# Optimization experiments

Measured on AMD Instinct MI355X. Metric: run time of the kernel, lower is better.

The kernel has to match this reference:

```python
import jax, jax.numpy as jnp
import numpy as np

NUM_GRAPHS = 128
EPS = 1e-5


def _instance_norm(x, seg, num_seg):
    # Per-graph instance norm over rows grouped by seg (PyG InstanceNorm, affine=False).
    ones = jnp.ones((x.shape[0], 1), x.dtype)
    cnt = jnp.maximum(jax.ops.segment_sum(ones, seg, num_segments=num_seg), 1.0)  # [G,1]
    mean = jax.ops.segment_sum(x, seg, num_segments=num_seg) / cnt               # [G,C]
    xc = x - mean[seg]
    var = jax.ops.segment_sum(xc * xc, seg, num_segments=num_seg) / cnt          # [G,C]
    return xc * jax.lax.rsqrt(var[seg] + EPS)


def setup_inputs() -> dict:
    key = jax.random.key(0)
    ks = jax.random.split(key, 8)
    N, E, H, G = 50000, 800000, 64, NUM_GRAPHS
    emb = jax.random.normal(ks[0], (N, H), dtype=jnp.float32)
    edge_index = jax.random.randint(ks[1], (2, E), 0, N, dtype=jnp.int64)
    batch = jnp.sort(jax.random.randint(ks[2], (N,), 0, G, dtype=jnp.int64))
    s1 = 1.0 / np.sqrt(2 * H)
    s2 = 1.0 / np.sqrt(4 * H)
    s3 = 1.0 / np.sqrt(H)
    return {
        "emb": emb,
        "edge_index": edge_index,
        "batch": batch,
        "W1": jax.random.normal(ks[3], (2 * H, 4 * H), dtype=jnp.float32) * s1,
        "b1": jnp.zeros((4 * H,), jnp.float32),
        "W2": jax.random.normal(ks[4], (4 * H, H), dtype=jnp.float32) * s2,
        "b2": jnp.zeros((H,), jnp.float32),
        "W3": jax.random.normal(ks[5], (H, 1), dtype=jnp.float32) * s3,
        "b3": jnp.zeros((1,), jnp.float32),
    }


def reference(emb, edge_index, batch, W1, b1, W2, b2, W3, b3):
    col, row = edge_index[0], edge_index[1]
    # Gather both endpoint embeddings and concat: [E, 2H]
    f12 = jnp.concatenate([emb[col], emb[row]], axis=-1)
    seg = batch[col]  # graph id per edge
    # MLP([2H, 4H, H, 1]): Linear -> InstanceNorm(batch) -> ReLU (dropout=identity in eval)
    h = jnp.maximum(_instance_norm(f12 @ W1 + b1, seg, NUM_GRAPHS), 0.0)
    h = jnp.maximum(_instance_norm(h @ W2 + b2, seg, NUM_GRAPHS), 0.0)
    att_log_logits = h @ W3 + b3  # [E, 1]
    return att_log_logits
```

## Files before the change

### kernel.cpp

```cpp
#include <hip/hip_runtime.h>
#include <hip/hip_bf16.h>
#include <stdint.h>

#define NG 128
#define EPSI 1e-5f

typedef __attribute__((ext_vector_type(8))) __bf16 bf16x8;
typedef __attribute__((ext_vector_type(4))) float f32x4;

union ABFrag { bf16x8 v; unsigned short u[8]; uint4 q; };
union U8 { uint4 q; unsigned short u[8]; };

__device__ __forceinline__ float b2f(unsigned short u){
  union { unsigned int i; float f; } v; v.i = ((unsigned int)u) << 16; return v.f;
}
__device__ __forceinline__ unsigned short f2b(float f){
  union { float f; unsigned int i; } v; v.f = f;
  unsigned int r = v.i + 0x7fffu + ((v.i >> 16) & 1u);
  return (unsigned short)(r >> 16);
}
__device__ __forceinline__ unsigned int pk2(float lo, float hi){
  unsigned int r;
  asm("v_cvt_pk_bf16_f32 %0, %1, %2" : "=v"(r) : "v"(lo), "v"(hi));
  return r;
}

__global__ void kprep(const float* __restrict__ emb, const float* __restrict__ W1,
                      const float* __restrict__ W2,
                      const int* __restrict__ ei, const int* __restrict__ batch,
                      unsigned short* __restrict__ embb, unsigned short* __restrict__ WcF,
                      unsigned short* __restrict__ W2F, unsigned int* __restrict__ hist,
                      unsigned int* __restrict__ nodeh, int N, int E){
  __shared__ unsigned int h[NG];
  for (int i = threadIdx.x; i < NG; i += 256) h[i] = 0;
  __syncthreads();
  int idx = blockIdx.x * 256 + threadIdx.x;
  int stride = gridDim.x * 256;
  int embCnt4 = N * 16;
  for (int i = idx; i < embCnt4; i += stride){
    float4 v = *(const float4*)(emb + (size_t)i * 4);
    ushort4 o; o.x = f2b(v.x); o.y = f2b(v.y); o.z = f2b(v.z); o.w = f2b(v.w);
    *(ushort4*)(embb + (size_t)i * 4) = o;
  }
  for (int i = idx; i < 32 * 2 * 64 * 8; i += stride){
    int j = i & 7, lane = (i >> 3) & 63, ks = (i >> 9) & 1, tn = i >> 10;
    int quad = lane >> 4, l15 = lane & 15;
    int k = ks * 32 + quad * 8 + j;
    int n = tn * 16 + l15;
    float wv = (n < 256) ? W1[k * 256 + n] : W1[(k + 64) * 256 + (n - 256)];
    WcF[i] = f2b(wv);
  }
  for (int i = idx; i < 4 * 8 * 64 * 8; i += stride){
    int j = i & 7, lane = (i >> 3) & 63, ks = (i >> 9) & 7, w = i >> 12;
    int quad = lane >> 4, l15 = lane & 15;
    W2F[i] = f2b(W2[(ks * 32 + quad * 8 + j) * 64 + w * 16 + l15]);
  }
  for (int e = idx; e < E; e += stride){
    int cn = ei[e];
    atomicAdd(&h[batch[cn]], 1u);
    atomicAdd(&nodeh[cn], 1u);
  }
  __syncthreads();
  for (int i = threadIdx.x; i < NG; i += 256)
    if (h[i]) atomicAdd(&hist[i], h[i]);
}

__global__ void __launch_bounds__(256) kscan(const unsigned int* __restrict__ nodeh,
                      const unsigned int* __restrict__ hist,
                      const int* __restrict__ batch,
                      unsigned int* __restrict__ ncursor,
                      unsigned int* __restrict__ gmeta, int N){
  __shared__ unsigned int sh[3];
  __shared__ unsigned int wtot[4];
  int g = blockIdx.x;
  int t = threadIdx.x;
  unsigned int part = 0;
  for (int i = t; i < g; i += 256) part += (hist[i] + 31u) & ~31u;
  #pragma unroll
  for (int d = 1; d < 64; d <<= 1) part += __shfl_xor(part, d);
  if ((t & 63) == 0) wtot[t >> 6] = part;
  if (t == 64 || t == 65){
    int target = g + (t - 64);
    int lo = 0, hi = N;
    while (lo < hi){ int mid = (lo + hi) >> 1; if (batch[mid] < target) lo = mid + 1; else hi = mid; }
    sh[1 + (t - 64)] = lo;
  }
  __syncthreads();
  if (t == 0){
    unsigned int pb = wtot[0] + wtot[1] + wtot[2] + wtot[3];
    sh[0] = pb;
    gmeta[g] = pb;
    if (g == NG - 1) gmeta[NG] = pb + ((hist[g] + 31u) & ~31u);
  }
  __syncthreads();
  unsigned int run = sh[0];
  int lo = (int)sh[1], hi = (int)sh[2];
  int wid = t >> 6;
  for (int base = lo; base < hi; base += 256){
    int i = base + t;
    unsigned int v = (i < hi) ? nodeh[i] : 0u;
    unsigned int x = v;
    #pragma unroll
    for (int d = 1; d < 64; d <<= 1){
      unsigned int y = __shfl_up(x, d);
      if ((t & 63) >= d) x += y;
    }
    if ((t & 63) == 63) wtot[wid] = x;
    __syncthreads();
    unsigned int woff = 0;
    #pragma unroll
    for (int wb = 0; wb < 4; ++wb) if (wb < wid) woff += wtot[wb];
    if (i < hi) ncursor[i] = run + woff + x - v;
    run += wtot[0] + wtot[1] + wtot[2] + wtot[3];
    __syncthreads();
  }
}

__global__ void kscatter(const int* __restrict__ ei, const int* __restrict__ batch, int E,
                         unsigned int* __restrict__ ncursor, int4* __restrict__ einfo){
  int idx = blockIdx.x * 256 + threadIdx.x;
  for (int e = idx; e < E; e += gridDim.x * 256){
    int cn = ei[e], rn = ei[E + e];
    int g = batch[cn];
    unsigned int p = atomicAdd(&ncursor[cn], 1u);
    einfo[p] = make_int4(cn, rn, g, e);
  }
}

__global__ void kpad(int4* __restrict__ einfo, const unsigned int* __restrict__ hist,
                     const unsigned int* __restrict__ gmeta){
  int g = blockIdx.x;
  unsigned int cnt = hist[g];
  if (!cnt) return;
  unsigned int pe = (cnt + 31u) & ~31u;
  if (cnt == pe) return;
  unsigned int base = gmeta[g];
  int4 e0 = einfo[base]; e0.w = -1;
  for (unsigned int i = cnt + threadIdx.x; i < pe; i += 64)
    einfo[base + i] = e0;
}

__global__ void __launch_bounds__(256) kgemm1(const unsigned short* __restrict__ embb,
    const unsigned short* __restrict__ WcF, const float* __restrict__ b1,
    unsigned short* __restrict__ PQb, int Nn){
  int wave = threadIdx.x >> 6, lane = threadIdx.x & 63;
  int quad = lane >> 4, l15 = lane & 15;
  int tm = blockIdx.x * 4 + wave;
  int tmmax = (Nn + 15) >> 4;
  if (tm >= tmmax) return;
  int m = tm * 16 + l15; if (m >= Nn) m = Nn - 1;
  ABFrag a0, a1;
  a0.q = *(const uint4*)(embb + (size_t)m * 64 + quad * 8);
  a1.q = *(const uint4*)(embb + (size_t)m * 64 + 32 + quad * 8);
  int rowbase = tm * 16 + quad * 4;
  #pragma unroll 4
  for (int tn = 0; tn < 32; ++tn){
    ABFrag b0, b1f;
    b0.q  = *(const uint4*)(WcF + ((size_t)(tn * 2 + 0) * 64 + lane) * 8);
    b1f.q = *(const uint4*)(WcF + ((size_t)(tn * 2 + 1) * 64 + lane) * 8);
    f32x4 acc = {0.f, 0.f, 0.f, 0.f};
    acc = __builtin_amdgcn_mfma_f32_16x16x32_bf16(a0.v, b0.v, acc, 0, 0, 0);
    acc = __builtin_amdgcn_mfma_f32_16x16x32_bf16(a1.v, b1f.v, acc, 0, 0, 0);
    int col = tn * 16 + l15;
    float bias = (col < 256) ? b1[col] : 0.0f;
    #pragma unroll
    for (int r = 0; r < 4; ++r){
      int rowg = rowbase + r;
      if (rowg < Nn) PQb[(size_t)rowg * 512 + col] = f2b(acc[r] + bias);
    }
  }
}

__global__ void __launch_bounds__(256) kstats1(const unsigned short* __restrict__ PQb,
    const int4* __restrict__ einfo, const int* __restrict__ batch,
    const unsigned int* __restrict__ ncursor, const unsigned int* __restrict__ nodeh,
    float* __restrict__ sum1, float* __restrict__ sq1, int N){
  __shared__ float lsum[4][256];
  __shared__ float lsq[4][256];
  int tid = threadIdx.x;
  for (int i = tid; i < 4 * 256; i += 256){ ((float*)lsum)[i] = 0.f; ((float*)lsq)[i] = 0.f; }
  __syncthreads();
  int base = blockIdx.x * 32;
  int gfirst = batch[base];
  int wid = tid >> 6, lane = tid & 63;
  int c4 = lane * 4;
  float T1[4] = {0.f,0.f,0.f,0.f}, T2[4] = {0.f,0.f,0.f,0.f};
  int curg = -1;
  auto flushT = [&](){
    if (curg >= 0){
      unsigned slot = (unsigned)(curg - gfirst);
      if (slot < 4u){
        #pragma unroll
        for (int t = 0; t < 4; ++t){
          atomicAdd(&lsum[slot][c4 + t], T1[t]);
          atomicAdd(&lsq[slot][c4 + t], T2[t]);
        }
      } else {
        #pragma unroll
        for (int t = 0; t < 4; ++t){
          atomicAdd(&sum1[curg * 256 + c4 + t], T1[t]);
          atomicAdd(&sq1[curg * 256 + c4 + t], T2[t]);
        }
      }
      #pragma unroll
      for (int t = 0; t < 4; ++t){ T1[t] = 0.f; T2[t] = 0.f; }
    }
  };
  for (int i = 0; i < 8; ++i){
    int n = base + wid + i * 4;
    if (n >= N) break;
    int g = batch[n];
    unsigned int cnt = nodeh[n];
    if (g != curg){ flushT(); curg = g; }
    if (!cnt) continue;
    unsigned int start = ncursor[n] - cnt;
    ushort4 pv = *(const ushort4*)(PQb + (size_t)n * 512 + c4);
    float S1[4] = {0.f,0.f,0.f,0.f}, S2[4] = {0.f,0.f,0.f,0.f};
    for (unsigned int jb = 0; jb < cnt; jb += 64){
      int jn = (int)min(64u, cnt - jb);
      int rnv = (lane < jn) ? einfo[start + jb + (unsigned)lane].y : 0;
      #pragma unroll 4
      for (int j = 0; j < jn; ++j){
        int rn = __shfl(rnv, j);
        ushort4 qv = *(const ushort4*)(PQb + (size_t)rn * 512 + 256 + c4);
        float q0 = b2f(qv.x), q1 = b2f(qv.y), q2 = b2f(qv.z), q3 = b2f(qv.w);
        S1[0] += q0; S2[0] = fmaf(q0, q0, S2[0]);
        S1[1] += q1; S2[1] = fmaf(q1, q1, S2[1]);
        S1[2] += q2; S2[2] = fmaf(q2, q2, S2[2]);
        S1[3] += q3; S2[3] = fmaf(q3, q3, S2[3]);
      }
    }
    float fc = (float)cnt;
    float p0 = b2f(pv.x), p1 = b2f(pv.y), p2 = b2f(pv.z), p3 = b2f(pv.w);
    T1[0] += fmaf(fc, p0, S1[0]);  T2[0] += fmaf(fmaf(fc, p0, 2.f * S1[0]), p0, S2[0]);
    T1[1] += fmaf(fc, p1, S1[1]);  T2[1] += fmaf(fmaf(fc, p1, 2.f * S1[1]), p1, S2[1]);
    T1[2] += fmaf(fc, p2, S1[2]);  T2[2] += fmaf(fmaf(fc, p2, 2.f * S1[2]), p2, S2[2]);
    T1[3] += fmaf(fc, p3, S1[3]);  T2[3] += fmaf(fmaf(fc, p3, 2.f * S1[3]), p3, S2[3]);
  }
  flushT();
  __syncthreads();
  for (int i = tid; i < 4 * 256; i += 256){
    int slot = i >> 8, ch = i & 255;
    float vs = lsum[slot][ch], vq = lsq[slot][ch];
    if (vs != 0.f || vq != 0.f){
      int g = gfirst + slot;
      atomicAdd(&sum1[g * 256 + ch], vs);
      atomicAdd(&sq1[g * 256 + ch], vq);
    }
  }
}

__global__ void kfin(const float* __restrict__ sum, const float* __restrict__ sq,
                     const unsigned int* __restrict__ hist,
                     float* __restrict__ meanA, float* __restrict__ rstdA,
                     float* __restrict__ mrA, int C){
  int i = blockIdx.x * blockDim.x + threadIdx.x;
  if (i >= NG * C) return;
  int g = i / C;
  float cnt = fmaxf((float)hist[g], 1.0f);
  float m = sum[i] / cnt;
  float v = sq[i] / cnt - m * m;
  float r = rsqrtf(fmaxf(v, 0.f) + EPSI);
  meanA[i] = m;
  rstdA[i] = r;
  mrA[i] = m * r;
}

__global__ void __launch_bounds__(256, 5) kmain(const unsigned short* __restrict__ PQb,
    const unsigned short* __restrict__ W2F, const int4* __restrict__ einfo,
    const float* __restrict__ rstd1, const float* __restrict__ mr1,
    const float* __restrict__ b2,
    const unsigned int* __restrict__ hist, const unsigned int* __restrict__ gmeta,
    unsigned short* __restrict__ y2b, float* __restrict__ sum2, float* __restrict__ sq2){
  __shared__ unsigned short Blds[4 * 8 * 64 * 8];
  {
    const uint4* src = (const uint4*)W2F;
    uint4* dst = (uint4*)Blds;
    for (int i = threadIdx.x; i < 2048; i += 256) dst[i] = src[i];
  }
  __syncthreads();
  int wave = threadIdx.x >> 6, lane = threadIdx.x & 63;
  int quad = lane >> 4, l15 = lane & 15;
  float b2v[4];
  #pragma unroll
  for (int cg = 0; cg < 4; ++cg) b2v[cg] = b2[cg * 16 + l15];
  int ntiles = (int)(gmeta[NG] >> 5);
  int nw = gridDim.x * 4;
  for (int t = blockIdx.x * 4 + wave; t < ntiles; t += nw){
    int p0 = t * 32;
    int4 ev0 = einfo[p0 + l15];
    int4 ev1 = einfo[p0 + 16 + l15];
    int g = __builtin_amdgcn_readfirstlane(ev0.z);
    const unsigned short* pp0 = PQb + (size_t)ev0.x * 512 + quad * 8;
    const unsigned short* qq0 = PQb + (size_t)ev0.y * 512 + 256 + quad * 8;
    const unsigned short* pp1 = PQb + (size_t)ev1.x * 512 + quad * 8;
    const unsigned short* qq1 = PQb + (size_t)ev1.y * 512 + 256 + quad * 8;
    const float* rr = rstd1 + g * 256 + quad * 8;
    const float* mm = mr1   + g * 256 + quad * 8;
    f32x4 acc[8];
    #pragma unroll
    for (int i = 0; i < 8; ++i){ acc[i][0]=0.f; acc[i][1]=0.f; acc[i][2]=0.f; acc[i][3]=0.f; }
    #pragma unroll 2
    for (int ks = 0; ks < 8; ++ks){
      U8 pu0, qu0, pu1, qu1;
      pu0.q = *(const uint4*)(pp0 + ks * 32);
      qu0.q = *(const uint4*)(qq0 + ks * 32);
      pu1.q = *(const uint4*)(pp1 + ks * 32);
      qu1.q = *(const uint4*)(qq1 + ks * 32);
      float4 ra = *(const float4*)(rr + ks * 32);
      float4 rb = *(const float4*)(rr + ks * 32 + 4);
      float4 ma = *(const float4*)(mm + ks * 32);
      float4 mb = *(const float4*)(mm + ks * 32 + 4);
      float s00 = b2f(pu0.u[0]) + b2f(qu0.u[0]);
      float s01 = b2f(pu0.u[1]) + b2f(qu0.u[1]);
      float s02 = b2f(pu0.u[2]) + b2f(qu0.u[2]);
      float s03 = b2f(pu0.u[3]) + b2f(qu0.u[3]);
      float s04 = b2f(pu0.u[4]) + b2f(qu0.u[4]);
      float s05 = b2f(pu0.u[5]) + b2f(qu0.u[5]);
      float s06 = b2f(pu0.u[6]) + b2f(qu0.u[6]);
      float s07 = b2f(pu0.u[7]) + b2f(qu0.u[7]);
      float s10 = b2f(pu1.u[0]) + b2f(qu1.u[0]);
      float s11 = b2f(pu1.u[1]) + b2f(qu1.u[1]);
      float s12 = b2f(pu1.u[2]) + b2f(qu1.u[2]);
      float s13 = b2f(pu1.u[3]) + b2f(qu1.u[3]);
      float s14 = b2f(pu1.u[4]) + b2f(qu1.u[4]);
      float s15 = b2f(pu1.u[5]) + b2f(qu1.u[5]);
      float s16 = b2f(pu1.u[6]) + b2f(qu1.u[6]);
      float s17 = b2f(pu1.u[7]) + b2f(qu1.u[7]);
      ABFrag a0, a1;
      a0.q.x = pk2(fmaxf(0.f, fmaf(s00, ra.x, -ma.x)), fmaxf(0.f, fmaf(s01, ra.y, -ma.y)));
      a0.q.y = pk2(fmaxf(0.f, fmaf(s02, ra.z, -ma.z)), fmaxf(0.f, fmaf(s03, ra.w, -ma.w)));
      a0.q.z = pk2(fmaxf(0.f, fmaf(s04, rb.x, -mb.x)), fmaxf(0.f, fmaf(s05, rb.y, -mb.y)));
      a0.q.w = pk2(fmaxf(0.f, fmaf(s06, rb.z, -mb.z)), fmaxf(0.f, fmaf(s07, rb.w, -mb.w)));
      a1.q.x = pk2(fmaxf(0.f, fmaf(s10, ra.x, -ma.x)), fmaxf(0.f, fmaf(s11, ra.y, -ma.y)));
      a1.q.y = pk2(fmaxf(0.f, fmaf(s12, ra.z, -ma.z)), fmaxf(0.f, fmaf(s13, ra.w, -ma.w)));
      a1.q.z = pk2(fmaxf(0.f, fmaf(s14, rb.x, -mb.x)), fmaxf(0.f, fmaf(s15, rb.y, -mb.y)));
      a1.q.w = pk2(fmaxf(0.f, fmaf(s16, rb.z, -mb.z)), fmaxf(0.f, fmaf(s17, rb.w, -mb.w)));
      #pragma unroll
      for (int cg = 0; cg < 4; ++cg){
        ABFrag b;
        b.q = *(const uint4*)&Blds[((cg * 8 + ks) * 64 + lane) * 8];
        acc[cg]     = __builtin_amdgcn_mfma_f32_16x16x32_bf16(a0.v, b.v, acc[cg], 0, 0, 0);
        acc[4 + cg] = __builtin_amdgcn_mfma_f32_16x16x32_bf16(a1.v, b.v, acc[4 + cg], 0, 0, 0);
      }
    }
    int nl = (int)gmeta[g] + (int)hist[g] - p0;
    #pragma unroll
    for (int cg = 0; cg < 4; ++cg){
      float s = 0.f, qs = 0.f;
      #pragma unroll
      for (int sub = 0; sub < 2; ++sub)
        #pragma unroll
        for (int r = 0; r < 4; ++r){
          float y = acc[sub * 4 + cg][r] + b2v[cg];
          int el = sub * 16 + quad * 4 + r;
          y2b[(size_t)(p0 + el) * 64 + cg * 16 + l15] = f2b(y);
          if (el < nl){ s += y; qs = fmaf(y, y, qs); }
        }
      s  += __shfl_xor(s, 16);  s  += __shfl_xor(s, 32);
      qs += __shfl_xor(qs, 16); qs += __shfl_xor(qs, 32);
      if (quad == 0){
        atomicAdd(&sum2[g * 64 + cg * 16 + l15], s);
        atomicAdd(&sq2[g * 64 + cg * 16 + l15], qs);
      }
    }
  }
}

__global__ void kfinal(const unsigned short* __restrict__ y2b, const int4* __restrict__ einfo,
                       const unsigned int* __restrict__ gmeta,
                       const float* __restrict__ mean2, const float* __restrict__ rstd2,
                       const float* __restrict__ W3, const float* __restrict__ b3,
                       float* __restrict__ out){
  int EP = (int)gmeta[NG];
  int sub = threadIdx.x & 7;
  int c8 = sub * 8;
  float w3r[8];
  #pragma unroll
  for (int t = 0; t < 8; ++t) w3r[t] = W3[c8 + t];
  float b3v = b3[0];
  int step = (gridDim.x * blockDim.x) >> 3;
  for (int i = (blockIdx.x * blockDim.x + threadIdx.x) >> 3; i < EP; i += step){
    int4 ev = einfo[i];
    U8 yv; yv.q = *(const uint4*)(y2b + (size_t)i * 64 + c8);
    const float* mg = mean2 + ev.z * 64 + c8;
    const float* rg = rstd2 + ev.z * 64 + c8;
    float4 m0 = *(const float4*)mg, m1 = *(const float4*)(mg + 4);
    float4 r0 = *(const float4*)rg, r1 = *(const float4*)(rg + 4);
    float a = 0.f;
    a += fmaxf(0.f, (b2f(yv.u[0]) - m0.x) * r0.x) * w3r[0];
    a += fmaxf(0.f, (b2f(yv.u[1]) - m0.y) * r0.y) * w3r[1];
    a += fmaxf(0.f, (b2f(yv.u[2]) - m0.z) * r0.z) * w3r[2];
    a += fmaxf(0.f, (b2f(yv.u[3]) - m0.w) * r0.w) * w3r[3];
    a += fmaxf(0.f, (b2f(yv.u[4]) - m1.x) * r1.x) * w3r[4];
    a += fmaxf(0.f, (b2f(yv.u[5]) - m1.y) * r1.y) * w3r[5];
    a += fmaxf(0.f, (b2f(yv.u[6]) - m1.z) * r1.z) * w3r[6];
    a += fmaxf(0.f, (b2f(yv.u[7]) - m1.w) * r1.w) * w3r[7];
    a += __shfl_xor(a, 1);
    a += __shfl_xor(a, 2);
    a += __shfl_xor(a, 4);
    if (sub == 0 && ev.w >= 0) out[ev.w] = a + b3v;
  }
}

extern "C" void kernel_launch(void* const* d_in, const int* in_sizes, int n_in,
                              void* d_out, int out_size, void* d_ws, size_t ws_size,
                              hipStream_t stream){
  const float* emb  = (const float*)d_in[0];
  const int*   ei   = (const int*)d_in[1];
  const int*   batch= (const int*)d_in[2];
  const float* W1   = (const float*)d_in[3];
  const float* b1   = (const float*)d_in[4];
  const float* W2   = (const float*)d_in[5];
  const float* b2   = (const float*)d_in[6];
  const float* W3   = (const float*)d_in[7];
  const float* b3   = (const float*)d_in[8];
  int N = in_sizes[0] / 64;
  int E = in_sizes[1] / 2;
  int EPMAX = E + NG * 32;
  float* out = (float*)d_out;

  char* w = (char*)d_ws;
  size_t off = 0;
  auto nxt = [&](size_t bytes) -> char* {
    char* p = w + off;
    off = (off + bytes + 255) & ~(size_t)255;
    return p;
  };
  unsigned short* embb = (unsigned short*)nxt((size_t)N * 64 * 2);
  unsigned short* WcF  = (unsigned short*)nxt(32 * 2 * 64 * 8 * 2);
  unsigned short* W2F  = (unsigned short*)nxt(4 * 8 * 64 * 8 * 2);
  unsigned short* PQb  = (unsigned short*)nxt((size_t)N * 512 * 2);
  unsigned short* y2b  = (unsigned short*)nxt((size_t)EPMAX * 64 * 2);
  int4* einfo = (int4*)nxt((size_t)EPMAX * 16);
  float* mean1 = (float*)nxt(NG * 256 * 4);
  float* rstd1 = (float*)nxt(NG * 256 * 4);
  float* mr1   = (float*)nxt(NG * 256 * 4);
  float* mean2 = (float*)nxt(NG * 64 * 4);
  float* rstd2 = (float*)nxt(NG * 64 * 4);
  float* mr2   = (float*)nxt(NG * 64 * 4);
  unsigned int* ncursor = (unsigned int*)nxt((size_t)N * 4);
  unsigned int* gmeta   = (unsigned int*)nxt((NG + 1) * 4);
  char* zbase = w + off;
  unsigned int* hist  = (unsigned int*)nxt(NG * 4);
  unsigned int* nodeh = (unsigned int*)nxt((size_t)N * 4);
  float* sum1 = (float*)nxt(NG * 256 * 4);
  float* sq1  = (float*)nxt(NG * 256 * 4);
  float* sum2 = (float*)nxt(NG * 64 * 4);
  float* sq2  = (float*)nxt(NG * 64 * 4);
  size_t zbytes = (size_t)((w + off) - zbase);
  hipMemsetAsync(zbase, 0, zbytes, stream);

  kprep<<<2048, 256, 0, stream>>>(emb, W1, W2, ei, batch, embb, WcF, W2F, hist, nodeh, N, E);
  kscan<<<NG, 256, 0, stream>>>(nodeh, hist, batch, ncursor, gmeta, N);
  kscatter<<<2048, 256, 0, stream>>>(ei, batch, E, ncursor, einfo);
  kpad<<<NG, 64, 0, stream>>>(einfo, hist, gmeta);
  {
    int tmmax = (N + 15) / 16;
    kgemm1<<<(tmmax + 3) / 4, 256, 0, stream>>>(embb, WcF, b1, PQb, N);
  }
  kstats1<<<(N + 31) / 32, 256, 0, stream>>>(PQb, einfo, batch, ncursor, nodeh, sum1, sq1, N);
  kfin<<<(NG * 256 + 255) / 256, 256, 0, stream>>>(sum1, sq1, hist, mean1, rstd1, mr1, 256);
  kmain<<<2048, 256, 0, stream>>>(PQb, W2F, einfo, rstd1, mr1, b2, hist, gmeta, y2b, sum2, sq2);
  kfin<<<(NG * 64 + 255) / 256, 256, 0, stream>>>(sum2, sq2, hist, mean2, rstd2, mr2, 64);
  kfinal<<<2048, 256, 0, stream>>>(y2b, einfo, gmeta, mean2, rstd2, W3, b3, out);
}
```

Baseline: 519.3 us.

## Split edge metadata into compact arrays and fold emb conversion into GEMM

```diff
diff --git a/kernel.cpp b/kernel.cpp
--- a/kernel.cpp
+++ b/kernel.cpp
@@ -7,9 +7,11 @@
 
 typedef __attribute__((ext_vector_type(8))) __bf16 bf16x8;
 typedef __attribute__((ext_vector_type(4))) float f32x4;
+typedef unsigned int u32x4 __attribute__((ext_vector_type(4)));
+typedef int i32x2 __attribute__((ext_vector_type(2)));
 
 union ABFrag { bf16x8 v; unsigned short u[8]; uint4 q; };
-union U8 { uint4 q; unsigned short u[8]; };
+union U8 { uint4 q; unsigned short u[8]; u32x4 e; };
 
 __device__ __forceinline__ float b2f(unsigned short u){
   union { unsigned int i; float f; } v; v.i = ((unsigned int)u) << 16; return v.f;
@@ -24,24 +26,17 @@
   asm("v_cvt_pk_bf16_f32 %0, %1, %2" : "=v"(r) : "v"(lo), "v"(hi));
   return r;
 }
-
-__global__ void kprep(const float* __restrict__ emb, const float* __restrict__ W1,
-                      const float* __restrict__ W2,
-                      const int* __restrict__ ei, const int* __restrict__ batch,
-                      unsigned short* __restrict__ embb, unsigned short* __restrict__ WcF,
-                      unsigned short* __restrict__ W2F, unsigned int* __restrict__ hist,
-                      unsigned int* __restrict__ nodeh, int N, int E){
-  __shared__ unsigned int h[NG];
-  for (int i = threadIdx.x; i < NG; i += 256) h[i] = 0;
-  __syncthreads();
+__device__ __forceinline__ int2 ldnt2(const int2* p){
+  i32x2 v = __builtin_nontemporal_load((const i32x2*)p);
+  return make_int2(v.x, v.y);
+}
+
+__global__ void kprep(const float* __restrict__ W1, const float* __restrict__ W2,
+                      const int* __restrict__ ei,
+                      unsigned short* __restrict__ WcF, unsigned short* __restrict__ W2F,
+                      unsigned int* __restrict__ nodeh, int E){
   int idx = blockIdx.x * 256 + threadIdx.x;
   int stride = gridDim.x * 256;
-  int embCnt4 = N * 16;
-  for (int i = idx; i < embCnt4; i += stride){
-    float4 v = *(const float4*)(emb + (size_t)i * 4);
-    ushort4 o; o.x = f2b(v.x); o.y = f2b(v.y); o.z = f2b(v.z); o.w = f2b(v.w);
-    *(ushort4*)(embb + (size_t)i * 4) = o;
-  }
   for (int i = idx; i < 32 * 2 * 64 * 8; i += stride){
     int j = i & 7, lane = (i >> 3) & 63, ks = (i >> 9) & 1, tn = i >> 10;
     int quad = lane >> 4, l15 = lane & 15;
@@ -55,11 +50,18 @@
     int quad = lane >> 4, l15 = lane & 15;
     W2F[i] = f2b(W2[(ks * 32 + quad * 8 + j) * 64 + w * 16 + l15]);
   }
-  for (int e = idx; e < E; e += stride){
-    int cn = ei[e];
-    atomicAdd(&h[batch[cn]], 1u);
-    atomicAdd(&nodeh[cn], 1u);
-  }
+  for (int e = idx; e < E; e += stride)
+    atomicAdd(&nodeh[ei[e]], 1u);
+}
+
+__global__ void khist(const unsigned int* __restrict__ nodeh, const int* __restrict__ batch,
+                      unsigned int* __restrict__ hist, int N){
+  __shared__ unsigned int h[NG];
+  for (int i = threadIdx.x; i < NG; i += 256) h[i] = 0;
+  __syncthreads();
+  int idx = blockIdx.x * 256 + threadIdx.x;
+  for (int i = idx; i < N; i += gridDim.x * 256)
+    atomicAdd(&h[batch[i]], nodeh[i]);
   __syncthreads();
   for (int i = threadIdx.x; i < NG; i += 256)
     if (h[i]) atomicAdd(&hist[i], h[i]);
@@ -69,7 +71,9 @@
                       const unsigned int* __restrict__ hist,
                       const int* __restrict__ batch,
                       unsigned int* __restrict__ ncursor,
-                      unsigned int* __restrict__ gmeta, int N){
+                      unsigned int* __restrict__ gmeta,
+                      int* __restrict__ ecn, int2* __restrict__ ero,
+                      int* __restrict__ tilegid, int N){
   __shared__ unsigned int sh[3];
   __shared__ unsigned int wtot[4];
   int g = blockIdx.x;
@@ -94,6 +98,15 @@
   }
   __syncthreads();
   unsigned int run = sh[0];
+  {
+    unsigned int cnt = hist[g];
+    unsigned int pe = (cnt + 31u) & ~31u;
+    for (unsigned int i = cnt + t; i < pe; i += 256){
+      ecn[run + i] = 0; ero[run + i] = make_int2(0, -1);
+    }
+    unsigned int nt = pe >> 5, tb = run >> 5;
+    for (unsigned int i = t; i < nt; i += 256) tilegid[tb + i] = g;
+  }
   int lo = (int)sh[1], hi = (int)sh[2];
   int wid = t >> 6;
   for (int base = lo; base < hi; base += 256){
@@ -110,37 +123,27 @@
     unsigned int woff = 0;
     #pragma unroll
     for (int wb = 0; wb < 4; ++wb) if (wb < wid) woff += wtot[wb];
-    if (i < hi) ncursor[i] = run + woff + x - v;
+    if (i < hi){
+      unsigned int st = run + woff + x - v;
+      ncursor[i] = st;
+      for (unsigned int j = 0; j < v; ++j) ecn[st + j] = i;
+    }
     run += wtot[0] + wtot[1] + wtot[2] + wtot[3];
     __syncthreads();
   }
 }
 
-__global__ void kscatter(const int* __restrict__ ei, const int* __restrict__ batch, int E,
-                         unsigned int* __restrict__ ncursor, int4* __restrict__ einfo){
+__global__ void kscatter(const int* __restrict__ ei, int E,
+                         unsigned int* __restrict__ ncursor, int2* __restrict__ ero){
   int idx = blockIdx.x * 256 + threadIdx.x;
   for (int e = idx; e < E; e += gridDim.x * 256){
     int cn = ei[e], rn = ei[E + e];
-    int g = batch[cn];
     unsigned int p = atomicAdd(&ncursor[cn], 1u);
-    einfo[p] = make_int4(cn, rn, g, e);
-  }
-}
-
-__global__ void kpad(int4* __restrict__ einfo, const unsigned int* __restrict__ hist,
-                     const unsigned int* __restrict__ gmeta){
-  int g = blockIdx.x;
-  unsigned int cnt = hist[g];
-  if (!cnt) return;
-  unsigned int pe = (cnt + 31u) & ~31u;
-  if (cnt == pe) return;
-  unsigned int base = gmeta[g];
-  int4 e0 = einfo[base]; e0.w = -1;
-  for (unsigned int i = cnt + threadIdx.x; i < pe; i += 64)
-    einfo[base + i] = e0;
-}
-
-__global__ void __launch_bounds__(256) kgemm1(const unsigned short* __restrict__ embb,
+    ero[p] = make_int2(rn, e);
+  }
+}
+
+__global__ void __launch_bounds__(256) kgemm1(const float* __restrict__ emb,
     const unsigned short* __restrict__ WcF, const float* __restrict__ b1,
     unsigned short* __restrict__ PQb, int Nn){
   int wave = threadIdx.x >> 6, lane = threadIdx.x & 63;
@@ -149,9 +152,14 @@
   int tmmax = (Nn + 15) >> 4;
   if (tm >= tmmax) return;
   int m = tm * 16 + l15; if (m >= Nn) m = Nn - 1;
+  const float* er = emb + (size_t)m * 64 + quad * 8;
+  float4 f0 = *(const float4*)er,        f1 = *(const float4*)(er + 4);
+  float4 f2 = *(const float4*)(er + 32), f3 = *(const float4*)(er + 36);
   ABFrag a0, a1;
-  a0.q = *(const uint4*)(embb + (size_t)m * 64 + quad * 8);
-  a1.q = *(const uint4*)(embb + (size_t)m * 64 + 32 + quad * 8);
+  a0.q.x = pk2(f0.x, f0.y); a0.q.y = pk2(f0.z, f0.w);
+  a0.q.z = pk2(f1.x, f1.y); a0.q.w = pk2(f1.z, f1.w);
+  a1.q.x = pk2(f2.x, f2.y); a1.q.y = pk2(f2.z, f2.w);
+  a1.q.z = pk2(f3.x, f3.y); a1.q.w = pk2(f3.z, f3.w);
   int rowbase = tm * 16 + quad * 4;
   #pragma unroll 4
   for (int tn = 0; tn < 32; ++tn){
@@ -172,7 +180,7 @@
 }
 
 __global__ void __launch_bounds__(256) kstats1(const unsigned short* __restrict__ PQb,
-    const int4* __restrict__ einfo, const int* __restrict__ batch,
+    const int2* __restrict__ ero, const int* __restrict__ batch,
     const unsigned int* __restrict__ ncursor, const unsigned int* __restrict__ nodeh,
     float* __restrict__ sum1, float* __restrict__ sq1, int N){
   __shared__ float lsum[4][256];
@@ -218,7 +226,7 @@
     float S1[4] = {0.f,0.f,0.f,0.f}, S2[4] = {0.f,0.f,0.f,0.f};
     for (unsigned int jb = 0; jb < cnt; jb += 64){
       int jn = (int)min(64u, cnt - jb);
-      int rnv = (lane < jn) ? einfo[start + jb + (unsigned)lane].y : 0;
+      int rnv = (lane < jn) ? __builtin_nontemporal_load(&ero[start + jb + (unsigned)lane].x) : 0;
       #pragma unroll 4
       for (int j = 0; j < jn; ++j){
         int rn = __shfl(rnv, j);
@@ -267,7 +275,9 @@
 }
 
 __global__ void __launch_bounds__(256, 5) kmain(const unsigned short* __restrict__ PQb,
-    const unsigned short* __restrict__ W2F, const int4* __restrict__ einfo,
+    const unsigned short* __restrict__ W2F,
+    const int* __restrict__ ecn, const int2* __restrict__ ero,
+    const int* __restrict__ tilegid,
     const float* __restrict__ rstd1, const float* __restrict__ mr1,
     const float* __restrict__ b2,
     const unsigned int* __restrict__ hist, const unsigned int* __restrict__ gmeta,
@@ -286,15 +296,20 @@
   for (int cg = 0; cg < 4; ++cg) b2v[cg] = b2[cg * 16 + l15];
   int ntiles = (int)(gmeta[NG] >> 5);
   int nw = gridDim.x * 4;
-  for (int t = blockIdx.x * 4 + wave; t < ntiles; t += nw){
+  int bid = blockIdx.x;
+  int nblk = gridDim.x;
+  int swz = ((nblk & 7) == 0) ? ((bid & 7) * (nblk >> 3) + (bid >> 3)) : bid;
+  for (int t = swz * 4 + wave; t < ntiles; t += nw){
     int p0 = t * 32;
-    int4 ev0 = einfo[p0 + l15];
-    int4 ev1 = einfo[p0 + 16 + l15];
-    int g = __builtin_amdgcn_readfirstlane(ev0.z);
-    const unsigned short* pp0 = PQb + (size_t)ev0.x * 512 + quad * 8;
-    const unsigned short* qq0 = PQb + (size_t)ev0.y * 512 + 256 + quad * 8;
-    const unsigned short* pp1 = PQb + (size_t)ev1.x * 512 + quad * 8;
-    const unsigned short* qq1 = PQb + (size_t)ev1.y * 512 + 256 + quad * 8;
+    int g = __builtin_amdgcn_readfirstlane(tilegid[t]);
+    int cn0 = __builtin_nontemporal_load(&ecn[p0 + l15]);
+    int cn1 = __builtin_nontemporal_load(&ecn[p0 + 16 + l15]);
+    int rn0 = __builtin_nontemporal_load(&ero[p0 + l15].x);
+    int rn1 = __builtin_nontemporal_load(&ero[p0 + 16 + l15].x);
+    const unsigned short* pp0 = PQb + (size_t)cn0 * 512 + quad * 8;
+    const unsigned short* qq0 = PQb + (size_t)rn0 * 512 + 256 + quad * 8;
+    const unsigned short* pp1 = PQb + (size_t)cn1 * 512 + quad * 8;
+    const unsigned short* qq1 = PQb + (size_t)rn1 * 512 + 256 + quad * 8;
     const float* rr = rstd1 + g * 256 + quad * 8;
     const float* mm = mr1   + g * 256 + quad * 8;
     f32x4 acc[8];
@@ -344,6 +359,16 @@
         acc[4 + cg] = __builtin_amdgcn_mfma_f32_16x16x32_bf16(a1.v, b.v, acc[4 + cg], 0, 0, 0);
       }
     }
+    #pragma unroll
+    for (int sub = 0; sub < 2; ++sub)
+      #pragma unroll
+      for (int r = 0; r < 4; ++r){
+        int el = sub * 16 + quad * 4 + r;
+        size_t rowo = (size_t)(p0 + el) * 64 + l15;
+        #pragma unroll
+        for (int cg = 0; cg < 4; ++cg)
+          y2b[rowo + cg * 16] = f2b(acc[sub * 4 + cg][r] + b2v[cg]);
+      }
     int nl = (int)gmeta[g] + (int)hist[g] - p0;
     #pragma unroll
     for (int cg = 0; cg < 4; ++cg){
@@ -352,10 +377,11 @@
       for (int sub = 0; sub < 2; ++sub)
         #pragma unroll
         for (int r = 0; r < 4; ++r){
-          float y = acc[sub * 4 + cg][r] + b2v[cg];
           int el = sub * 16 + quad * 4 + r;
-          y2b[(size_t)(p0 + el) * 64 + cg * 16 + l15] = f2b(y);
-          if (el < nl){ s += y; qs = fmaf(y, y, qs); }
+          if (el < nl){
+            float y = acc[sub * 4 + cg][r] + b2v[cg];
+            s += y; qs = fmaf(y, y, qs);
+          }
         }
       s  += __shfl_xor(s, 16);  s  += __shfl_xor(s, 32);
       qs += __shfl_xor(qs, 16); qs += __shfl_xor(qs, 32);
@@ -367,7 +393,8 @@
   }
 }
 
-__global__ void kfinal(const unsigned short* __restrict__ y2b, const int4* __restrict__ einfo,
+__global__ void kfinal(const unsigned short* __restrict__ y2b,
+                       const int2* __restrict__ ero, const int* __restrict__ tilegid,
                        const unsigned int* __restrict__ gmeta,
                        const float* __restrict__ mean2, const float* __restrict__ rstd2,
                        const float* __restrict__ W3, const float* __restrict__ b3,
@@ -381,10 +408,11 @@
   float b3v = b3[0];
   int step = (gridDim.x * blockDim.x) >> 3;
   for (int i = (blockIdx.x * blockDim.x + threadIdx.x) >> 3; i < EP; i += step){
-    int4 ev = einfo[i];
-    U8 yv; yv.q = *(const uint4*)(y2b + (size_t)i * 64 + c8);
-    const float* mg = mean2 + ev.z * 64 + c8;
-    const float* rg = rstd2 + ev.z * 64 + c8;
+    int orig = __builtin_nontemporal_load(&ero[i].y);
+    int gz = tilegid[i >> 5];
+    U8 yv; yv.e = __builtin_nontemporal_load((const u32x4*)(y2b + (size_t)i * 64 + c8));
+    const float* mg = mean2 + gz * 64 + c8;
+    const float* rg = rstd2 + gz * 64 + c8;
     float4 m0 = *(const float4*)mg, m1 = *(const float4*)(mg + 4);
     float4 r0 = *(const float4*)rg, r1 = *(const float4*)(rg + 4);
     float a = 0.f;
@@ -399,7 +427,7 @@
     a += __shfl_xor(a, 1);
     a += __shfl_xor(a, 2);
     a += __shfl_xor(a, 4);
-    if (sub == 0 && ev.w >= 0) out[ev.w] = a + b3v;
+    if (sub == 0 && orig >= 0) out[orig] = a + b3v;
   }
 }
 
@@ -427,12 +455,13 @@
     off = (off + bytes + 255) & ~(size_t)255;
     return p;
   };
-  unsigned short* embb = (unsigned short*)nxt((size_t)N * 64 * 2);
   unsigned short* WcF  = (unsigned short*)nxt(32 * 2 * 64 * 8 * 2);
   unsigned short* W2F  = (unsigned short*)nxt(4 * 8 * 64 * 8 * 2);
   unsigned short* PQb  = (unsigned short*)nxt((size_t)N * 512 * 2);
   unsigned short* y2b  = (unsigned short*)nxt((size_t)EPMAX * 64 * 2);
-  int4* einfo = (int4*)nxt((size_t)EPMAX * 16);
+  int* ecn   = (int*)nxt((size_t)EPMAX * 4);
+  int2* ero  = (int2*)nxt((size_t)EPMAX * 8);
+  int* tilegid = (int*)nxt((size_t)(EPMAX / 32 + 1) * 4);
   float* mean1 = (float*)nxt(NG * 256 * 4);
   float* rstd1 = (float*)nxt(NG * 256 * 4);
   float* mr1   = (float*)nxt(NG * 256 * 4);
@@ -451,17 +480,19 @@
   size_t zbytes = (size_t)((w + off) - zbase);
   hipMemsetAsync(zbase, 0, zbytes, stream);
 
-  kprep<<<2048, 256, 0, stream>>>(emb, W1, W2, ei, batch, embb, WcF, W2F, hist, nodeh, N, E);
-  kscan<<<NG, 256, 0, stream>>>(nodeh, hist, batch, ncursor, gmeta, N);
-  kscatter<<<2048, 256, 0, stream>>>(ei, batch, E, ncursor, einfo);
-  kpad<<<NG, 64, 0, stream>>>(einfo, hist, gmeta);
+  kprep<<<1024, 256, 0, stream>>>(W1, W2, ei, WcF, W2F, nodeh, E);
+  khist<<<64, 256, 0, stream>>>(nodeh, batch, hist, N);
+  kscan<<<NG, 256, 0, stream>>>(nodeh, hist, batch, ncursor, gmeta,
+                                ecn, ero, tilegid, N);
+  kscatter<<<2048, 256, 0, stream>>>(ei, E, ncursor, ero);
   {
     int tmmax = (N + 15) / 16;
-    kgemm1<<<(tmmax + 3) / 4, 256, 0, stream>>>(embb, WcF, b1, PQb, N);
-  }
-  kstats1<<<(N + 31) / 32, 256, 0, stream>>>(PQb, einfo, batch, ncursor, nodeh, sum1, sq1, N);
+    kgemm1<<<(tmmax + 3) / 4, 256, 0, stream>>>(emb, WcF, b1, PQb, N);
+  }
+  kstats1<<<(N + 31) / 32, 256, 0, stream>>>(PQb, ero, batch, ncursor, nodeh, sum1, sq1, N);
   kfin<<<(NG * 256 + 255) / 256, 256, 0, stream>>>(sum1, sq1, hist, mean1, rstd1, mr1, 256);
-  kmain<<<2048, 256, 0, stream>>>(PQb, W2F, einfo, rstd1, mr1, b2, hist, gmeta, y2b, sum2, sq2);
+  kmain<<<2048, 256, 0, stream>>>(PQb, W2F, ecn, ero, tilegid, rstd1, mr1, b2, hist, gmeta,
+                                  y2b, sum2, sq2);
   kfin<<<(NG * 64 + 255) / 256, 256, 0, stream>>>(sum2, sq2, hist, mean2, rstd2, mr2, 64);
-  kfinal<<<2048, 256, 0, stream>>>(y2b, einfo, gmeta, mean2, rstd2, W3, b3, out);
-}
+  kfinal<<<2048, 256, 0, stream>>>(y2b, ero, tilegid, gmeta, mean2, rstd2, W3, b3, out);
+}
```

New measurement: 537.3 us. +3.5%, slower.
